# Kernel tuning notes

Hardware: AMD Instinct MI355X
Metric: run time of the kernel (lower is better)

## Reference

```python
import jax, jax.numpy as jnp
import numpy as np
import math

B, S, D = 1, 2048, 4096
H, H_KV, HD = 32, 8, 128  # n_heads, n_kv_heads, head_dim; n_rep = H // H_KV


def setup_inputs() -> dict:
    key = jax.random.key(0)
    ks = jax.random.split(key, 6)
    sc = lambda fan_in: 1.0 / math.sqrt(fan_in)
    x = jax.random.normal(ks[0], (B, S, D), jnp.float32)
    wq = jax.random.normal(ks[1], (D, H * HD), jnp.float32) * sc(D)
    wk = jax.random.normal(ks[2], (D, H_KV * HD), jnp.float32) * sc(D)
    wv = jax.random.normal(ks[3], (D, H_KV * HD), jnp.float32) * sc(D)
    wo = jax.random.normal(ks[4], (H * HD, D), jnp.float32) * sc(H * HD)
    # rotary frequencies: theta=10000, angles[t, j] = t / 10000^(2j/HD)
    inv_freq = 1.0 / (10000.0 ** (np.arange(0, HD, 2, dtype=np.float32) / HD))
    t = np.arange(S, dtype=np.float32)
    ang = np.outer(t, inv_freq)  # (S, HD/2)
    freqs_cos = jnp.asarray(np.cos(ang))
    freqs_sin = jnp.asarray(np.sin(ang))
    # causal additive mask (0 on/below diagonal, -1e9 above)
    causal = np.triu(np.full((S, S), -1e9, dtype=np.float32), k=1)
    mask = jnp.asarray(causal)[None, None]  # (1,1,S,S)
    return {"x": x, "wq": wq, "wk": wk, "wv": wv, "wo": wo,
            "freqs_cos": freqs_cos, "freqs_sin": freqs_sin, "mask": mask,
            "start_pos": 0, "init_seqlen": S}


def _rope(t, cos, sin):
    # t: (B, S, h, HD); even/odd interleaved pairs form complex numbers
    t0, t1 = t[..., 0::2], t[..., 1::2]
    c = cos[None, :, None, :]
    s = sin[None, :, None, :]
    o0 = t0 * c - t1 * s
    o1 = t0 * s + t1 * c
    return jnp.stack([o0, o1], axis=-1).reshape(t.shape)


def reference(x, wq, wk, wv, wo, freqs_cos, freqs_sin, mask, start_pos, init_seqlen):
    bsz, seqlen, _ = x.shape
    n_rep = H // H_KV
    xq = (x @ wq).reshape(bsz, seqlen, H, HD)
    xk = (x @ wk).reshape(bsz, seqlen, H_KV, HD)
    xv = (x @ wv).reshape(bsz, seqlen, H_KV, HD)
    xq = _rope(xq, freqs_cos[-seqlen:], freqs_sin[-seqlen:])
    xk = _rope(xk, freqs_cos[-seqlen:], freqs_sin[-seqlen:])
    # prefill branch (init_seqlen != 1) with T_fade >= init_seqlen:
    # fade_start = 0, cache[0:init_seqlen] = xk/xv, so keys/values == xk/xv.
    keys = jnp.repeat(xk, n_rep, axis=2)    # (B, S, H, HD) GQA repeat_kv
    values = jnp.repeat(xv, n_rep, axis=2)
    scores = jnp.einsum('bqhd,bkhd->bhqk', xq, keys) / math.sqrt(HD)
    scores = scores + mask[:, :, -seqlen:, -seqlen:]
    attn = jax.nn.softmax(scores.astype(jnp.float32), axis=-1).astype(xq.dtype)
    out = jnp.einsum('bhqk,bkhd->bqhd', attn, values).reshape(bsz, seqlen, H * HD)
    return out @ wo
```

## Files before the change

### kernel.cpp

```cpp
#include <hip/hip_runtime.h>

#define S_LEN 2048
#define D_MODEL 4096
#define N_HEADS 32
#define N_KV 8
#define HEAD_DIM 128

typedef float f32x4 __attribute__((ext_vector_type(4)));
typedef short bf16x8 __attribute__((ext_vector_type(8)));

__device__ __forceinline__ unsigned short f2bf(float f) {
  unsigned int u = __float_as_uint(f);
  unsigned int r = (u + 0x7fffu + ((u >> 16) & 1u)) >> 16;
  return (unsigned short)r;
}
__device__ __forceinline__ float bf2f(unsigned short b) {
  return __uint_as_float(((unsigned int)b) << 16);
}
__device__ __forceinline__ void gload_lds16(const void* g, void* l) {
  __builtin_amdgcn_global_load_lds((const __attribute__((address_space(1))) void*)g,
                                   (__attribute__((address_space(3))) void*)l, 16, 0, 0);
}

__global__ void cvt_f32_bf16(const float* __restrict__ in, unsigned short* __restrict__ out, int n4) {
  int stride = gridDim.x * blockDim.x;
  for (int i = blockIdx.x * blockDim.x + threadIdx.x; i < n4; i += stride) {
    float4 v = ((const float4*)in)[i];
    unsigned int lo = (unsigned int)f2bf(v.x) | ((unsigned int)f2bf(v.y) << 16);
    unsigned int hi = (unsigned int)f2bf(v.z) | ((unsigned int)f2bf(v.w) << 16);
    uint2 o; o.x = lo; o.y = hi;
    ((uint2*)out)[i] = o;
  }
}

__global__ void transpose_cvt(const float* __restrict__ in, unsigned short* __restrict__ out,
                              int K, int N) {
  __shared__ float tile[32][33];
  int k0 = blockIdx.y << 5, n0 = blockIdx.x << 5;
  int tx = threadIdx.x, ty = threadIdx.y;
#pragma unroll
  for (int r = 0; r < 32; r += 8)
    tile[ty + r][tx] = in[(k0 + ty + r) * N + n0 + tx];
  __syncthreads();
#pragma unroll
  for (int r = 0; r < 32; r += 8)
    out[(n0 + ty + r) * K + k0 + tx] = f2bf(tile[tx][ty + r]);
}

__global__ void transpose_bf16(const unsigned short* __restrict__ in, unsigned short* __restrict__ out,
                               int inStride, int outStride, int col0) {
  __shared__ unsigned short tile[32][33];
  int r0 = blockIdx.y << 5, c0 = blockIdx.x << 5;
  int tx = threadIdx.x, ty = threadIdx.y;
#pragma unroll
  for (int r = 0; r < 32; r += 8)
    tile[ty + r][tx] = in[(r0 + ty + r) * inStride + col0 + c0 + tx];
  __syncthreads();
#pragma unroll
  for (int r = 0; r < 32; r += 8)
    out[(c0 + ty + r) * outStride + r0 + tx] = tile[tx][ty + r];
}

__global__ void rope_k(unsigned short* __restrict__ t, const float* __restrict__ cb,
                       const float* __restrict__ sb, int rowStride, int shift) {
  int idx = blockIdx.x * blockDim.x + threadIdx.x;
  int pos = idx >> shift;
  int wp = idx & ((1 << shift) - 1);
  int p = wp & 63;
  int col = ((wp >> 6) << 7) + (p << 1);
  unsigned int* addr = (unsigned int*)&t[pos * rowStride + col];
  unsigned int pr = *addr;
  float t0 = bf2f((unsigned short)(pr & 0xffffu));
  float t1 = bf2f((unsigned short)(pr >> 16));
  float c = cb[pos * 64 + p], s = sb[pos * 64 + p];
  float o0 = t0 * c - t1 * s;
  float o1 = t0 * s + t1 * c;
  *addr = (unsigned int)f2bf(o0) | ((unsigned int)f2bf(o1) << 16);
}

__device__ __forceinline__ void store_out(unsigned short* p, float v) { *p = f2bf(v); }
__device__ __forceinline__ void store_out(float* p, float v) { *p = v; }

template <typename OT>
__global__ __launch_bounds__(256, 2) void gemm_bt(const unsigned short* __restrict__ A,
                                                  const unsigned short* __restrict__ Bt,
                                                  OT* __restrict__ C, int M, int N, int K) {
  __shared__ __align__(16) unsigned short As[128 * 32];
  __shared__ __align__(16) unsigned short Bs[128 * 32];
  const int tid = threadIdx.x;
  const int w = tid >> 6, l = tid & 63;
  const int lrow = l & 15, lk = l >> 4;
  const int m0 = blockIdx.y * 128, n0 = blockIdx.x * 128;
  const int wm = (w >> 1) * 64, wn = (w & 1) * 64;
  f32x4 acc[4][4] = {};

  for (int kt = 0; kt < K; kt += 32) {
    __syncthreads();
#pragma unroll
    for (int p = 0; p < 2; ++p) {
      int e = (p * 256 + tid) * 8;
      int r = e >> 5, c = e & 31;
      gload_lds16(&A[(m0 + r) * K + kt + c], (char*)As + p * 4096 + w * 1024);
      gload_lds16(&Bt[(n0 + r) * K + kt + c], (char*)Bs + p * 4096 + w * 1024);
    }
    __syncthreads();
    bf16x8 af[4], bfr[4];
#pragma unroll
    for (int i = 0; i < 4; ++i)
      af[i] = *(const bf16x8*)&As[(wm + i * 16 + lrow) * 32 + lk * 8];
#pragma unroll
    for (int j = 0; j < 4; ++j)
      bfr[j] = *(const bf16x8*)&Bs[(wn + j * 16 + lrow) * 32 + lk * 8];
#pragma unroll
    for (int i = 0; i < 4; ++i)
#pragma unroll
      for (int j = 0; j < 4; ++j)
        acc[i][j] = __builtin_amdgcn_mfma_f32_16x16x32_bf16(af[i], bfr[j], acc[i][j], 0, 0, 0);
  }
#pragma unroll
  for (int i = 0; i < 4; ++i)
#pragma unroll
    for (int j = 0; j < 4; ++j)
#pragma unroll
      for (int r = 0; r < 4; ++r) {
        int row = m0 + wm + i * 16 + lk * 4 + r;
        int col = n0 + wn + j * 16 + lrow;
        store_out(&C[row * N + col], acc[i][j][r]);
      }
}

__global__ __launch_bounds__(256, 2) void attn_fwd(const unsigned short* __restrict__ Q,
                                                   const unsigned short* __restrict__ Kb,
                                                   const unsigned short* __restrict__ Vt,
                                                   unsigned short* __restrict__ Ctx) {
  __shared__ __align__(16) unsigned short Ks[64 * 128];
  __shared__ __align__(16) unsigned short Vs[128 * 64];
  __shared__ __align__(16) unsigned short Ps[4][32 * 72];

  const int tid = threadIdx.x, w = tid >> 6, l = tid & 63;
  const int lrow = l & 15, lk = l >> 4;
  const int qh = blockIdx.y;
  const int g = qh >> 2;
  const int qbi = gridDim.x - 1 - blockIdx.x;
  const int q0 = qbi * 128;
  const int wq0 = q0 + w * 32;
  const float scale = 0.08838834764831845f;
  const int kvStride = N_KV * HEAD_DIM;
  (void)kvStride;

  bf16x8 qf[2][4];
#pragma unroll
  for (int i = 0; i < 2; ++i)
#pragma unroll
    for (int ks = 0; ks < 4; ++ks)
      qf[i][ks] = *(const bf16x8*)&Q[(wq0 + i * 16 + lrow) * D_MODEL + qh * HEAD_DIM + ks * 32 + lk * 8];

  f32x4 o[2][8] = {};
  float mrun[2][4], lrun[2][4], al[2][4];
#pragma unroll
  for (int i = 0; i < 2; ++i)
#pragma unroll
    for (int r = 0; r < 4; ++r) { mrun[i][r] = -1e30f; lrun[i][r] = 0.0f; }

  const int nt = (q0 + 128) >> 6;
  for (int t = 0; t < nt; ++t) {
    const int kv0 = t << 6;
    __syncthreads();
#pragma unroll
    for (int p = 0; p < 4; ++p) {
      int o_b = p * 4096 + w * 1024 + (l << 4);
      int row = o_b >> 8;
      int sc = ((o_b >> 4) & 15) ^ (row & 7);
      gload_lds16(&Kb[(kv0 + row) * 2048 + g * HEAD_DIM + sc * 8],
                  (char*)Ks + p * 4096 + w * 1024);
    }
#pragma unroll
    for (int p = 0; p < 4; ++p) {
      int o_b = p * 4096 + w * 1024 + (l << 4);
      int row = o_b >> 7;
      int sc = ((o_b >> 4) & 7) ^ (row & 7);
      gload_lds16(&Vt[(g * HEAD_DIM + row) * 2048 + kv0 + sc * 8],
                  (char*)Vs + p * 4096 + w * 1024);
    }
    __syncthreads();

    f32x4 sa[2][4] = {};
#pragma unroll
    for (int ks = 0; ks < 4; ++ks) {
      bf16x8 kf[4];
#pragma unroll
      for (int j = 0; j < 4; ++j) {
        int row = j * 16 + lrow;
        kf[j] = *(const bf16x8*)&Ks[row * 128 + ((ks * 32 + lk * 8) ^ ((row & 7) << 3))];
      }
#pragma unroll
      for (int i = 0; i < 2; ++i)
#pragma unroll
        for (int j = 0; j < 4; ++j)
          sa[i][j] = __builtin_amdgcn_mfma_f32_16x16x32_bf16(qf[i][ks], kf[j], sa[i][j], 0, 0, 0);
    }

#pragma unroll
    for (int i = 0; i < 2; ++i)
#pragma unroll
      for (int r = 0; r < 4; ++r) {
        int qrow = wq0 + i * 16 + lk * 4 + r;
        float sv[4];
        float mx = -1e30f;
#pragma unroll
        for (int j = 0; j < 4; ++j) {
          float x = sa[i][j][r] * scale;
          int kvcol = kv0 + j * 16 + lrow;
          if (kvcol > qrow) x = -1e30f;
          sv[j] = x;
          mx = fmaxf(mx, x);
        }
#pragma unroll
        for (int d = 1; d < 16; d <<= 1) mx = fmaxf(mx, __shfl_xor(mx, d));
        float mold = mrun[i][r];
        float mnew = fmaxf(mold, mx);
        float alpha = __expf(mold - mnew);
        float rs = 0.0f;
        float ps[4];
#pragma unroll
        for (int j = 0; j < 4; ++j) { ps[j] = __expf(sv[j] - mnew); rs += ps[j]; }
#pragma unroll
        for (int d = 1; d < 16; d <<= 1) rs += __shfl_xor(rs, d);
        mrun[i][r] = mnew;
        lrun[i][r] = lrun[i][r] * alpha + rs;
        al[i][r] = alpha;
#pragma unroll
        for (int j = 0; j < 4; ++j)
          Ps[w][(i * 16 + lk * 4 + r) * 72 + j * 16 + lrow] = f2bf(ps[j]);
      }

#pragma unroll
    for (int i = 0; i < 2; ++i)
#pragma unroll
      for (int n = 0; n < 8; ++n)
#pragma unroll
        for (int r = 0; r < 4; ++r) o[i][n][r] *= al[i][r];

#pragma unroll
    for (int ks = 0; ks < 2; ++ks) {
      bf16x8 pa[2];
#pragma unroll
      for (int i = 0; i < 2; ++i)
        pa[i] = *(const bf16x8*)&Ps[w][(i * 16 + lrow) * 72 + ks * 32 + lk * 8];
#pragma unroll
      for (int n = 0; n < 8; ++n) {
        int row = n * 16 + lrow;
        bf16x8 vf = *(const bf16x8*)&Vs[row * 64 + ((ks * 32 + lk * 8) ^ ((row & 7) << 3))];
#pragma unroll
        for (int i = 0; i < 2; ++i)
          o[i][n] = __builtin_amdgcn_mfma_f32_16x16x32_bf16(pa[i], vf, o[i][n], 0, 0, 0);
      }
    }
  }

#pragma unroll
  for (int i = 0; i < 2; ++i) {
    float inv[4];
#pragma unroll
    for (int r = 0; r < 4; ++r) inv[r] = 1.0f / lrun[i][r];
#pragma unroll
    for (int n = 0; n < 8; ++n)
#pragma unroll
      for (int r = 0; r < 4; ++r) {
        int row = wq0 + i * 16 + lk * 4 + r;
        int col = n * 16 + lrow;
        Ctx[row * D_MODEL + qh * HEAD_DIM + col] = f2bf(o[i][n][r] * inv[r]);
      }
  }
}

extern "C" void kernel_launch(void* const* d_in, const int* in_sizes, int n_in,
                              void* d_out, int out_size, void* d_ws, size_t ws_size,
                              hipStream_t stream) {
  const float* x = (const float*)d_in[0];
  const float* wq = (const float*)d_in[1];
  const float* wk = (const float*)d_in[2];
  const float* wv = (const float*)d_in[3];
  const float* wo = (const float*)d_in[4];
  const float* fcos = (const float*)d_in[5];
  const float* fsin = (const float*)d_in[6];
  float* out = (float*)d_out;

  char* ws = (char*)d_ws;
  unsigned short* xb = (unsigned short*)ws;
  unsigned short* ctx = xb;
  unsigned short* wt = (unsigned short*)(ws + (size_t)16 * 1024 * 1024);
  unsigned short* qb = (unsigned short*)(ws + (size_t)48 * 1024 * 1024);
  unsigned short* kvb = (unsigned short*)(ws + (size_t)64 * 1024 * 1024);
  unsigned short* vtg = (unsigned short*)(ws + (size_t)72 * 1024 * 1024);

  cvt_f32_bf16<<<2048, 256, 0, stream>>>(x, xb, S_LEN * D_MODEL / 4);

  transpose_cvt<<<dim3(128, 128), dim3(32, 8), 0, stream>>>(wq, wt, 4096, 4096);
  gemm_bt<unsigned short><<<dim3(32, 16), 256, 0, stream>>>(xb, wt, qb, S_LEN, 4096, 4096);

  transpose_cvt<<<dim3(32, 128), dim3(32, 8), 0, stream>>>(wk, wt, 4096, 1024);
  transpose_cvt<<<dim3(32, 128), dim3(32, 8), 0, stream>>>(wv, wt + (size_t)1024 * 4096, 4096, 1024);
  gemm_bt<unsigned short><<<dim3(16, 16), 256, 0, stream>>>(xb, wt, kvb, S_LEN, 2048, 4096);

  rope_k<<<(S_LEN * 2048) / 256, 256, 0, stream>>>(qb, fcos, fsin, 4096, 11);
  rope_k<<<(S_LEN * 512) / 256, 256, 0, stream>>>(kvb, fcos, fsin, 2048, 9);

  transpose_bf16<<<dim3(32, 64), dim3(32, 8), 0, stream>>>(kvb, vtg, 2048, 2048, 1024);

  attn_fwd<<<dim3(S_LEN / 128, N_HEADS), 256, 0, stream>>>(qb, kvb, vtg, ctx);

  transpose_cvt<<<dim3(128, 128), dim3(32, 8), 0, stream>>>(wo, wt, 4096, 4096);
  gemm_bt<float><<<dim3(32, 16), 256, 0, stream>>>(ctx, wt, out, S_LEN, 4096, 4096);
}
```

Measured before the change: 646.0 us.

## Make attention waves independent, loading K/V straight from global without LDS

```diff
diff --git a/kernel.cpp b/kernel.cpp
--- a/kernel.cpp
+++ b/kernel.cpp
@@ -133,20 +133,16 @@
                                                    const unsigned short* __restrict__ Kb,
                                                    const unsigned short* __restrict__ Vt,
                                                    unsigned short* __restrict__ Ctx) {
-  __shared__ __align__(16) unsigned short Ks[64 * 128];
-  __shared__ __align__(16) unsigned short Vs[128 * 64];
   __shared__ __align__(16) unsigned short Ps[4][32 * 72];
 
   const int tid = threadIdx.x, w = tid >> 6, l = tid & 63;
   const int lrow = l & 15, lk = l >> 4;
-  const int qh = blockIdx.y;
+  const int gw = blockIdx.x * 4 + w;
+  const int qh = gw & 31;
+  const int qc = 63 - (gw >> 5);
+  const int wq0 = qc * 32;
   const int g = qh >> 2;
-  const int qbi = gridDim.x - 1 - blockIdx.x;
-  const int q0 = qbi * 128;
-  const int wq0 = q0 + w * 32;
-  const float scale = 0.08838834764831845f;
-  const int kvStride = N_KV * HEAD_DIM;
-  (void)kvStride;
+  const float scale2 = 0.12751879f;
 
   bf16x8 qf[2][4];
 #pragma unroll
@@ -162,37 +158,18 @@
 #pragma unroll
     for (int r = 0; r < 4; ++r) { mrun[i][r] = -1e30f; lrun[i][r] = 0.0f; }
 
-  const int nt = (q0 + 128) >> 6;
+  const int nt = (wq0 + 95) >> 6;
   for (int t = 0; t < nt; ++t) {
     const int kv0 = t << 6;
-    __syncthreads();
-#pragma unroll
-    for (int p = 0; p < 4; ++p) {
-      int o_b = p * 4096 + w * 1024 + (l << 4);
-      int row = o_b >> 8;
-      int sc = ((o_b >> 4) & 15) ^ (row & 7);
-      gload_lds16(&Kb[(kv0 + row) * 2048 + g * HEAD_DIM + sc * 8],
-                  (char*)Ks + p * 4096 + w * 1024);
-    }
-#pragma unroll
-    for (int p = 0; p < 4; ++p) {
-      int o_b = p * 4096 + w * 1024 + (l << 4);
-      int row = o_b >> 7;
-      int sc = ((o_b >> 4) & 7) ^ (row & 7);
-      gload_lds16(&Vt[(g * HEAD_DIM + row) * 2048 + kv0 + sc * 8],
-                  (char*)Vs + p * 4096 + w * 1024);
-    }
-    __syncthreads();
+    const bool last = (t == nt - 1);
 
     f32x4 sa[2][4] = {};
 #pragma unroll
     for (int ks = 0; ks < 4; ++ks) {
       bf16x8 kf[4];
 #pragma unroll
-      for (int j = 0; j < 4; ++j) {
-        int row = j * 16 + lrow;
-        kf[j] = *(const bf16x8*)&Ks[row * 128 + ((ks * 32 + lk * 8) ^ ((row & 7) << 3))];
-      }
+      for (int j = 0; j < 4; ++j)
+        kf[j] = *(const bf16x8*)&Kb[(kv0 + j * 16 + lrow) * 2048 + g * HEAD_DIM + ks * 32 + lk * 8];
 #pragma unroll
       for (int i = 0; i < 2; ++i)
 #pragma unroll
@@ -204,26 +181,35 @@
     for (int i = 0; i < 2; ++i)
 #pragma unroll
       for (int r = 0; r < 4; ++r) {
-        int qrow = wq0 + i * 16 + lk * 4 + r;
         float sv[4];
         float mx = -1e30f;
-#pragma unroll
-        for (int j = 0; j < 4; ++j) {
-          float x = sa[i][j][r] * scale;
-          int kvcol = kv0 + j * 16 + lrow;
-          if (kvcol > qrow) x = -1e30f;
-          sv[j] = x;
-          mx = fmaxf(mx, x);
+        if (last) {
+          int qrow = wq0 + i * 16 + lk * 4 + r;
+#pragma unroll
+          for (int j = 0; j < 4; ++j) {
+            float x = sa[i][j][r] * scale2;
+            int kvcol = kv0 + j * 16 + lrow;
+            if (kvcol > qrow) x = -1e30f;
+            sv[j] = x;
+            mx = fmaxf(mx, x);
+          }
+        } else {
+#pragma unroll
+          for (int j = 0; j < 4; ++j) {
+            float x = sa[i][j][r] * scale2;
+            sv[j] = x;
+            mx = fmaxf(mx, x);
+          }
         }
 #pragma unroll
         for (int d = 1; d < 16; d <<= 1) mx = fmaxf(mx, __shfl_xor(mx, d));
         float mold = mrun[i][r];
         float mnew = fmaxf(mold, mx);
-        float alpha = __expf(mold - mnew);
+        float alpha = __builtin_exp2f(mold - mnew);
         float rs = 0.0f;
         float ps[4];
 #pragma unroll
-        for (int j = 0; j < 4; ++j) { ps[j] = __expf(sv[j] - mnew); rs += ps[j]; }
+        for (int j = 0; j < 4; ++j) { ps[j] = __builtin_exp2f(sv[j] - mnew); rs += ps[j]; }
 #pragma unroll
         for (int d = 1; d < 16; d <<= 1) rs += __shfl_xor(rs, d);
         mrun[i][r] = mnew;
@@ -249,8 +235,7 @@
         pa[i] = *(const bf16x8*)&Ps[w][(i * 16 + lrow) * 72 + ks * 32 + lk * 8];
 #pragma unroll
       for (int n = 0; n < 8; ++n) {
-        int row = n * 16 + lrow;
-        bf16x8 vf = *(const bf16x8*)&Vs[row * 64 + ((ks * 32 + lk * 8) ^ ((row & 7) << 3))];
+        bf16x8 vf = *(const bf16x8*)&Vt[(g * HEAD_DIM + n * 16 + lrow) * 2048 + kv0 + ks * 32 + lk * 8];
 #pragma unroll
         for (int i = 0; i < 2; ++i)
           o[i][n] = __builtin_amdgcn_mfma_f32_16x16x32_bf16(pa[i], vf, o[i][n], 0, 0, 0);
@@ -308,7 +293,7 @@
 
   transpose_bf16<<<dim3(32, 64), dim3(32, 8), 0, stream>>>(kvb, vtg, 2048, 2048, 1024);
 
-  attn_fwd<<<dim3(S_LEN / 128, N_HEADS), 256, 0, stream>>>(qb, kvb, vtg, ctx);
+  attn_fwd<<<dim3(512), 256, 0, stream>>>(qb, kvb, vtg, ctx);
 
   transpose_cvt<<<dim3(128, 128), dim3(32, 8), 0, stream>>>(wo, wt, 4096, 4096);
   gemm_bt<float><<<dim3(32, 16), 256, 0, stream>>>(ctx, wt, out, S_LEN, 4096, 4096);
```

New measurement: 705.3 us. 1.09x slower.

## Register-prefetch KV tiles and add lazy rescaling softmax with exp2 in attention

Applied to the files above, without the earlier changes.

```diff
diff --git a/kernel.cpp b/kernel.cpp
--- a/kernel.cpp
+++ b/kernel.cpp
@@ -144,9 +144,9 @@
   const int qbi = gridDim.x - 1 - blockIdx.x;
   const int q0 = qbi * 128;
   const int wq0 = q0 + w * 32;
-  const float scale = 0.08838834764831845f;
-  const int kvStride = N_KV * HEAD_DIM;
-  (void)kvStride;
+  const int tdiag = wq0 >> 6;
+  const float scale2 = 0.12751743f;
+  const int o_base = w * 1024 + (l << 4);
 
   bf16x8 qf[2][4];
 #pragma unroll
@@ -156,35 +156,45 @@
       qf[i][ks] = *(const bf16x8*)&Q[(wq0 + i * 16 + lrow) * D_MODEL + qh * HEAD_DIM + ks * 32 + lk * 8];
 
   f32x4 o[2][8] = {};
-  float mrun[2][4], lrun[2][4], al[2][4];
+  float mrun[2][4], lrun[2][4];
 #pragma unroll
   for (int i = 0; i < 2; ++i)
 #pragma unroll
     for (int r = 0; r < 4; ++r) { mrun[i][r] = -1e30f; lrun[i][r] = 0.0f; }
 
+  uint4 kreg[4], vreg[4];
+#define LOADT(tt)                                                                     \
+  do {                                                                                \
+    int kv0p = (tt) << 6;                                                             \
+    _Pragma("unroll") for (int c = 0; c < 4; ++c) {                                   \
+      int o_b = c * 4096 + o_base;                                                    \
+      int rw = o_b >> 8;                                                              \
+      int sck = ((o_b >> 4) & 15) ^ (rw & 7);                                         \
+      kreg[c] = *(const uint4*)&Kb[(kv0p + rw) * 2048 + g * HEAD_DIM + sck * 8];      \
+      int rv = o_b >> 7;                                                              \
+      int scv = ((o_b >> 4) & 7) ^ (rv & 7);                                          \
+      vreg[c] = *(const uint4*)&Vt[(g * HEAD_DIM + rv) * 2048 + kv0p + scv * 8];      \
+    }                                                                                 \
+  } while (0)
+
+  LOADT(0);
   const int nt = (q0 + 128) >> 6;
   for (int t = 0; t < nt; ++t) {
+    __syncthreads();
+#pragma unroll
+    for (int c = 0; c < 4; ++c) {
+      int o_b = c * 4096 + o_base;
+      *(uint4*)((char*)Ks + o_b) = kreg[c];
+      *(uint4*)((char*)Vs + o_b) = vreg[c];
+    }
+    if (t + 1 < nt) LOADT(t + 1);
+    __syncthreads();
+    if (t > tdiag) continue;
     const int kv0 = t << 6;
-    __syncthreads();
-#pragma unroll
-    for (int p = 0; p < 4; ++p) {
-      int o_b = p * 4096 + w * 1024 + (l << 4);
-      int row = o_b >> 8;
-      int sc = ((o_b >> 4) & 15) ^ (row & 7);
-      gload_lds16(&Kb[(kv0 + row) * 2048 + g * HEAD_DIM + sc * 8],
-                  (char*)Ks + p * 4096 + w * 1024);
-    }
-#pragma unroll
-    for (int p = 0; p < 4; ++p) {
-      int o_b = p * 4096 + w * 1024 + (l << 4);
-      int row = o_b >> 7;
-      int sc = ((o_b >> 4) & 7) ^ (row & 7);
-      gload_lds16(&Vt[(g * HEAD_DIM + row) * 2048 + kv0 + sc * 8],
-                  (char*)Vs + p * 4096 + w * 1024);
-    }
-    __syncthreads();
+    const bool dia = (t == tdiag);
 
     f32x4 sa[2][4] = {};
+    __builtin_amdgcn_s_setprio(1);
 #pragma unroll
     for (int ks = 0; ks < 4; ++ks) {
       bf16x8 kf[4];
@@ -199,48 +209,79 @@
         for (int j = 0; j < 4; ++j)
           sa[i][j] = __builtin_amdgcn_mfma_f32_16x16x32_bf16(qf[i][ks], kf[j], sa[i][j], 0, 0, 0);
     }
-
+    __builtin_amdgcn_s_setprio(0);
+
+    if (dia) {
+#pragma unroll
+      for (int i = 0; i < 2; ++i)
+#pragma unroll
+        for (int j = 0; j < 4; ++j) {
+          int kvcol = kv0 + j * 16 + lrow;
+#pragma unroll
+          for (int r = 0; r < 4; ++r) {
+            int qrow = wq0 + i * 16 + lk * 4 + r;
+            float x = sa[i][j][r] * scale2;
+            sa[i][j][r] = (kvcol > qrow) ? -1e30f : x;
+          }
+        }
+    } else {
+#pragma unroll
+      for (int i = 0; i < 2; ++i)
+#pragma unroll
+        for (int j = 0; j < 4; ++j)
+#pragma unroll
+          for (int r = 0; r < 4; ++r) sa[i][j][r] *= scale2;
+    }
+
+    float tmx[2][4];
+    float grow = -1e30f;
 #pragma unroll
     for (int i = 0; i < 2; ++i)
 #pragma unroll
       for (int r = 0; r < 4; ++r) {
-        int qrow = wq0 + i * 16 + lk * 4 + r;
-        float sv[4];
-        float mx = -1e30f;
-#pragma unroll
-        for (int j = 0; j < 4; ++j) {
-          float x = sa[i][j][r] * scale;
-          int kvcol = kv0 + j * 16 + lrow;
-          if (kvcol > qrow) x = -1e30f;
-          sv[j] = x;
-          mx = fmaxf(mx, x);
+        float mx = fmaxf(fmaxf(sa[i][0][r], sa[i][1][r]), fmaxf(sa[i][2][r], sa[i][3][r]));
+#pragma unroll
+        for (int d = 1; d < 16; d <<= 1) mx = fmaxf(mx, __shfl_xor(mx, d));
+        tmx[i][r] = mx;
+        grow = fmaxf(grow, mx - mrun[i][r]);
+      }
+    if (__any(grow > 8.0f)) {
+      float al[2][4];
+#pragma unroll
+      for (int i = 0; i < 2; ++i)
+#pragma unroll
+        for (int r = 0; r < 4; ++r) {
+          float mnew = fmaxf(mrun[i][r], tmx[i][r]);
+          float a = __builtin_exp2f(mrun[i][r] - mnew);
+          mrun[i][r] = mnew;
+          lrun[i][r] *= a;
+          al[i][r] = a;
         }
 #pragma unroll
-        for (int d = 1; d < 16; d <<= 1) mx = fmaxf(mx, __shfl_xor(mx, d));
-        float mold = mrun[i][r];
-        float mnew = fmaxf(mold, mx);
-        float alpha = __expf(mold - mnew);
+      for (int i = 0; i < 2; ++i)
+#pragma unroll
+        for (int n = 0; n < 8; ++n)
+#pragma unroll
+          for (int r = 0; r < 4; ++r) o[i][n][r] *= al[i][r];
+    }
+
+#pragma unroll
+    for (int i = 0; i < 2; ++i)
+#pragma unroll
+      for (int r = 0; r < 4; ++r) {
+        float ps[4];
         float rs = 0.0f;
-        float ps[4];
-#pragma unroll
-        for (int j = 0; j < 4; ++j) { ps[j] = __expf(sv[j] - mnew); rs += ps[j]; }
+#pragma unroll
+        for (int j = 0; j < 4; ++j) { ps[j] = __builtin_exp2f(sa[i][j][r] - mrun[i][r]); rs += ps[j]; }
 #pragma unroll
         for (int d = 1; d < 16; d <<= 1) rs += __shfl_xor(rs, d);
-        mrun[i][r] = mnew;
-        lrun[i][r] = lrun[i][r] * alpha + rs;
-        al[i][r] = alpha;
+        lrun[i][r] += rs;
 #pragma unroll
         for (int j = 0; j < 4; ++j)
           Ps[w][(i * 16 + lk * 4 + r) * 72 + j * 16 + lrow] = f2bf(ps[j]);
       }
 
-#pragma unroll
-    for (int i = 0; i < 2; ++i)
-#pragma unroll
-      for (int n = 0; n < 8; ++n)
-#pragma unroll
-        for (int r = 0; r < 4; ++r) o[i][n][r] *= al[i][r];
-
+    __builtin_amdgcn_s_setprio(1);
 #pragma unroll
     for (int ks = 0; ks < 2; ++ks) {
       bf16x8 pa[2];
@@ -256,7 +297,9 @@
           o[i][n] = __builtin_amdgcn_mfma_f32_16x16x32_bf16(pa[i], vf, o[i][n], 0, 0, 0);
       }
     }
+    __builtin_amdgcn_s_setprio(0);
   }
+#undef LOADT
 
 #pragma unroll
   for (int i = 0; i < 2; ++i) {
@@ -308,7 +351,7 @@
 
   transpose_bf16<<<dim3(32, 64), dim3(32, 8), 0, stream>>>(kvb, vtg, 2048, 2048, 1024);
 
-  attn_fwd<<<dim3(S_LEN / 128, N_HEADS), 256, 0, stream>>>(qb, kvb, vtg, ctx);
+  attn_fwd<<<dim3(16, 32), 256, 0, stream>>>(qb, kvb, vtg, ctx);
 
   transpose_cvt<<<dim3(128, 128), dim3(32, 8), 0, stream>>>(wo, wt, 4096, 4096);
   gemm_bt<float><<<dim3(32, 16), 256, 0, stream>>>(ctx, wt, out, S_LEN, 4096, 4096);
```

After: 741.1 us. +14.7%, slower.
